# Kernel optimization log

Hardware: AMD Instinct MI355X
Metric: run time of the kernel (lower is better)

The kernel has to match this reference:

```python
import jax, jax.numpy as jnp
import numpy as np

EPS = 1e-5

def _conv(x, w, pad):
    # NCHW conv, stride 1, no bias
    return jax.lax.conv_general_dilated(x, w, (1, 1), [(pad, pad), (pad, pad)],
                                        dimension_numbers=('NCHW', 'OIHW', 'NCHW'))

def _bn(x, g, b, m, v):
    # inference-mode BatchNorm2d folded to scale/shift
    s = g * jax.lax.rsqrt(v + EPS)
    return x * s[None, :, None, None] + (b - m * s)[None, :, None, None]

def _cbr(x, w, g, b, m, v):
    # convolution helper module: 3x3 conv (pad 1, no bias) + BN + ReLU
    return jax.nn.relu(_bn(_conv(x, w, 1), g, b, m, v))


def setup_inputs() -> dict:
    key = jax.random.key(0)
    ks = iter(jax.random.split(key, 40))
    dim, mid, B, H, W = 256, 128, 4, 128, 128
    def conv_w(shape):
        fan = shape[1] * shape[2] * shape[3]
        return jax.random.normal(next(ks), shape, jnp.float32) / np.float32(np.sqrt(fan))
    def bn_p(c):
        return (jax.random.normal(next(ks), (c,), jnp.float32) * 0.1 + 1.0,
                jax.random.normal(next(ks), (c,), jnp.float32) * 0.1,
                jax.random.normal(next(ks), (c,), jnp.float32) * 0.1,
                jax.random.uniform(next(ks), (c,), jnp.float32, 0.5, 1.5))
    x = jax.random.normal(next(ks), (B, dim, H, W), jnp.float32)
    w_p1 = conv_w((mid, dim, 3, 3)); g_p1, b_p1, m_p1, v_p1 = bn_p(mid)
    w_p2 = conv_w((mid, dim, 3, 3)); g_p2, b_p2, m_p2, v_p2 = bn_p(mid)
    w_pc = conv_w((dim, mid, 3, 3)); g_pb, b_pb, m_pb, v_pb = bn_p(dim)
    w_c1 = conv_w((dim, dim, 1, 1)); g_b1, b_b1, m_b1, v_b1 = bn_p(dim)
    w_c2 = conv_w((dim, dim, 3, 3)); g_c2, b_c2, m_c2, v_c2 = bn_p(dim)
    return dict(x=x,
                w_p1=w_p1, g_p1=g_p1, b_p1=b_p1, m_p1=m_p1, v_p1=v_p1,
                w_p2=w_p2, g_p2=g_p2, b_p2=b_p2, m_p2=m_p2, v_p2=v_p2,
                w_pc=w_pc, g_pb=g_pb, b_pb=b_pb, m_pb=m_pb, v_pb=v_pb,
                w_c1=w_c1, g_b1=g_b1, b_b1=b_b1, m_b1=m_b1, v_b1=v_b1,
                w_c2=w_c2, g_c2=g_c2, b_c2=b_c2, m_c2=m_c2, v_c2=v_c2)


def reference(x, w_p1, g_p1, b_p1, m_p1, v_p1,
              w_p2, g_p2, b_p2, m_p2, v_p2,
              w_pc, g_pb, b_pb, m_pb, v_pb,
              w_c1, g_b1, b_b1, m_b1, v_b1,
              w_c2, g_c2, b_c2, m_c2, v_c2):
    p1 = _cbr(x, w_p1, g_p1, b_p1, m_p1, v_p1)          # [B,128,H,W]
    top = jax.lax.cummax(p1, axis=2, reverse=True)       # TopPool: max over rows below
    p2 = _cbr(x, w_p2, g_p2, b_p2, m_p2, v_p2)          # [B,128,H,W]
    left = jax.lax.cummax(p2, axis=3, reverse=True)      # LeftPool: max over cols to the right
    p_bn1 = _bn(_conv(top + left, w_pc, 1), g_pb, b_pb, m_pb, v_pb)  # [B,dim,H,W]
    bn1 = _bn(_conv(x, w_c1, 0), g_b1, b_b1, m_b1, v_b1)             # 1x1 skip branch
    relu1 = jax.nn.relu(p_bn1 + bn1)
    return _cbr(relu1, w_c2, g_c2, b_c2, m_c2, v_c2)
```

## Files before the change

### kernel.cpp

```cpp
#include <hip/hip_runtime.h>
#include <hip/hip_bf16.h>

#define HH 128
#define WW 128
#define BB 4
#define NPIX 16384
#define EPSV 1e-5f

using bfrag = __attribute__((ext_vector_type(8))) short;
using f32x4 = __attribute__((ext_vector_type(4))) float;
using us8   = __attribute__((ext_vector_type(8))) unsigned short;

__device__ __forceinline__ float bf2f(ushort u) {
  union { unsigned int i; float f; } x; x.i = ((unsigned int)u) << 16; return x.f;
}
__device__ __forceinline__ ushort f2bf(float f) {
  union { float f; unsigned int i; } x; x.f = f;
  unsigned int r = x.i + 0x7fffu + ((x.i >> 16) & 1u);
  return (ushort)(r >> 16);
}

#define GLOAD16(gsrc, ldst) \
  __builtin_amdgcn_global_load_lds( \
      (const __attribute__((address_space(1))) unsigned int*)(gsrc), \
      (__attribute__((address_space(3))) unsigned int*)(ldst), 16, 0, 0)

template<int CIN1, int TAPS1, int CIN2, int TAPS2, int COUT, int EPI>
__global__ __launch_bounds__(256, 2)
void convgemm(const ushort* __restrict__ B1,
              const ushort* __restrict__ B2,
              const ushort* __restrict__ wR,
              const float*  __restrict__ tb,
              const float*  __restrict__ tb2,
              void*          __restrict__ outp,
              const ushort* __restrict__ zerop)
{
  __shared__ ushort lds[2][16384];
  const int h      = blockIdx.x;
  const int o_base = blockIdx.y * 128;
  const int b      = blockIdx.z;
  const int tid  = threadIdx.x;
  const int lane = tid & 63;
  const int wid  = tid >> 6;
  const int m0 = (wid >> 1) * 64;
  const int n0 = (wid & 1) * 64;
  constexpr int nch1 = CIN1 / 64;
  constexpr int nch2 = (CIN2 > 0) ? CIN2 / 64 : 0;
  constexpr int NCH  = TAPS1 * nch1 + TAPS2 * nch2;

  f32x4 acc[4][4];
  #pragma unroll
  for (int i = 0; i < 4; ++i)
    #pragma unroll
    for (int j = 0; j < 4; ++j) acc[i][j] = (f32x4){0.f, 0.f, 0.f, 0.f};

  int rowB[4], ro1[4], ro2[4];
  #pragma unroll
  for (int s = 0; s < 4; ++s) {
    const int boff = (wid * 4 + s) * 1024 + lane * 16;
    rowB[s] = boff >> 7;
    const int sl8 = ((((boff >> 4) & 7) ^ (rowB[s] & 7)) << 3);
    ro1[s] = rowB[s] * CIN1 + sl8;
    ro2[s] = (CIN2 > 0) ? rowB[s] * CIN2 + sl8 : 0;
  }
  const size_t B1base = (size_t)b * NPIX * CIN1;
  const size_t B2base = (CIN2 > 0) ? (size_t)b * NPIX * CIN2 : 0;

  auto stage = [&](int t, int buf) {
    char* base = (char*)&lds[buf][0];
    const ushort* wsrc = wR + ((size_t)t * COUT + o_base) * 64;
    const ushort* bch;
    int zr; bool oob, ph2;
    if (CIN2 == 0 || t < TAPS1 * nch1) {
      const int tap = t / nch1, ch = t - tap * nch1;
      const int dy = (TAPS1 == 9) ? tap / 3 - 1 : 0;
      const int dx = (TAPS1 == 9) ? tap - (tap / 3) * 3 - 1 : 0;
      const int hy = h + dy;
      oob = (hy < 0) | (hy >= HH);
      zr  = (dx < 0) ? 0 : ((dx > 0) ? 127 : -1);
      bch = B1 + B1base + (size_t)(hy * WW + dx) * CIN1 + ch * 64;
      ph2 = false;
    } else {
      const int ch = t - TAPS1 * nch1;
      oob = false; zr = -1;
      bch = B2 + B2base + (size_t)(h * WW) * CIN2 + ch * 64;
      ph2 = true;
    }
    #pragma unroll
    for (int s = 0; s < 4; ++s) {
      const int off = (wid * 4 + s) * 1024;
      GLOAD16((const char*)wsrc + off + lane * 16, base + off);
      const int roff = ph2 ? ro2[s] : ro1[s];
      const ushort* bs = (oob || rowB[s] == zr) ? zerop : (bch + roff);
      GLOAD16(bs, base + 16384 + off);
    }
  };

  stage(0, 0);
  int cur = 0;
  for (int t = 0; t < NCH; ++t) {
    if (t + 1 < NCH) {
      stage(t + 1, cur ^ 1);
      asm volatile("s_waitcnt vmcnt(8)" ::: "memory");
    } else {
      asm volatile("s_waitcnt vmcnt(0)" ::: "memory");
    }
    __builtin_amdgcn_s_barrier();
    __builtin_amdgcn_sched_barrier(0);
    const char* base = (const char*)&lds[cur][0];
    __builtin_amdgcn_s_setprio(1);
    #pragma unroll
    for (int kc = 0; kc < 2; ++kc) {
      const int sw = ((((kc << 2) | (lane >> 4)) ^ (lane & 7)) << 4);
      bfrag af[4], bfv[4];
      #pragma unroll
      for (int mf = 0; mf < 4; ++mf)
        af[mf] = *(const bfrag*)(base + (m0 + mf * 16 + (lane & 15)) * 128 + sw);
      #pragma unroll
      for (int nf = 0; nf < 4; ++nf)
        bfv[nf] = *(const bfrag*)(base + 16384 + (n0 + nf * 16 + (lane & 15)) * 128 + sw);
      #pragma unroll
      for (int mf = 0; mf < 4; ++mf)
        #pragma unroll
        for (int nf = 0; nf < 4; ++nf)
          acc[mf][nf] = __builtin_amdgcn_mfma_f32_16x16x32_bf16(
              af[mf], bfv[nf], acc[mf][nf], 0, 0, 0);
    }
    __builtin_amdgcn_s_setprio(0);
    __builtin_amdgcn_sched_barrier(0);
    __builtin_amdgcn_s_barrier();
    cur ^= 1;
  }

  if (EPI == 4) {
    ushort* ct = (ushort*)&lds[0][0];
    const int pl0 = n0 + (lane & 15);
    #pragma unroll
    for (int mf = 0; mf < 4; ++mf) {
      #pragma unroll
      for (int r = 0; r < 4; ++r) {
        const int ol = m0 + mf * 16 + (lane >> 4) * 4 + r;
        const int o  = o_base + ol;
        const float bias = tb[o] + tb2[o];
        #pragma unroll
        for (int nf = 0; nf < 4; ++nf)
          ct[(pl0 + nf * 16) * 136 + ol] =
              f2bf(fmaxf(acc[mf][nf][r] + bias, 0.f));
      }
    }
    __syncthreads();
    const int p  = tid >> 1;
    const int hf = tid & 1;
    ushort* dst = (ushort*)outp +
                  ((size_t)b * NPIX + h * WW + p) * 256 + o_base + hf * 64;
    const ushort* src = ct + p * 136 + hf * 64;
    #pragma unroll
    for (int j = 0; j < 8; ++j)
      *(us8*)(dst + j * 8) = *(const us8*)(src + j * 8);
    return;
  }

  const int pc0 = h * WW + n0 + (lane & 15);
  #pragma unroll
  for (int mf = 0; mf < 4; ++mf) {
    #pragma unroll
    for (int r = 0; r < 4; ++r) {
      const int o = o_base + m0 + mf * 16 + (lane >> 4) * 4 + r;
      const float bias = tb[o];
      #pragma unroll
      for (int nf = 0; nf < 4; ++nf) {
        const int p = pc0 + nf * 16;
        float v = fmaxf(acc[mf][nf][r] + bias, 0.f);
        const size_t oi = ((size_t)(b * COUT + o)) * NPIX + p;
        if (EPI == 0) ((ushort*)outp)[oi] = f2bf(v);
        else          ((float*)outp)[oi] = v;
      }
    }
  }
}

struct WSeg {
  const float *W, *g, *bb, *mm, *vv;
  ushort* dst; float* tb;
  int CIN, COUT, TAPS, o_off, cb, start, end;
};

__device__ __forceinline__ void wrepack_one(const WSeg& s, int e) {
  const int tap = e % s.TAPS;
  const int ci  = (e / s.TAPS) % s.CIN;
  const int o   = e / (s.TAPS * s.CIN);
  const int oi  = o + s.o_off;
  const float sc = s.g[o] * rsqrtf(s.vv[o] + EPSV);
  const int nch = s.CIN / 64;
  const int ch = ci >> 6, kl = ci & 63;
  const int slot = (kl >> 3) ^ (oi & 7);
  s.dst[(((size_t)((s.cb + tap * nch + ch) * s.COUT) + oi) << 6) +
        (slot << 3) + (kl & 7)] = f2bf(s.W[e] * sc);
  if (ci == 0 && tap == 0) s.tb[oi] = s.bb[o] - s.mm[o] * sc;
}

__global__ __launch_bounds__(256)
void wrepack_all(WSeg s0, WSeg s1, WSeg s2, WSeg s3, WSeg s4) {
  const int id = blockIdx.x * 256 + threadIdx.x;
  if (id < s0.end)      wrepack_one(s0, id - s0.start);
  else if (id < s1.end) wrepack_one(s1, id - s1.start);
  else if (id < s2.end) wrepack_one(s2, id - s2.start);
  else if (id < s3.end) wrepack_one(s3, id - s3.start);
  else if (id < s4.end) wrepack_one(s4, id - s4.start);
}

__global__ __launch_bounds__(256)
void repack_x(const float* __restrict__ x, ushort* __restrict__ xT)
{
  const int b  = blockIdx.z;
  const int cq = threadIdx.x >> 6;
  const int pg = threadIdx.x & 63;
  const int p0 = blockIdx.x * 256 + pg * 4;
  const size_t xb = (size_t)b * 256 * NPIX;
  ushort* ob = xT + ((size_t)b * NPIX + p0) * 256 + cq * 64;
  for (int cc = 0; cc < 64; cc += 8) {
    us8 v[4];
    #pragma unroll
    for (int j = 0; j < 8; ++j) {
      const float4 q = *(const float4*)&x[xb + (size_t)(cq * 64 + cc + j) * NPIX + p0];
      v[0][j] = f2bf(q.x); v[1][j] = f2bf(q.y);
      v[2][j] = f2bf(q.z); v[3][j] = f2bf(q.w);
    }
    #pragma unroll
    for (int k = 0; k < 4; ++k)
      *(us8*)(ob + (size_t)k * 256 + cc) = v[k];
  }
}

__global__ __launch_bounds__(256)
void sum_repack(const ushort* __restrict__ p12, ushort* __restrict__ sT)
{
  const int b  = blockIdx.z;
  const int cq = threadIdx.x >> 6;
  const int pg = threadIdx.x & 63;
  const int p0 = blockIdx.x * 256 + pg * 4;
  const size_t base = (size_t)b * 256 * NPIX;
  const ushort* P1 = p12 + base;
  const ushort* P2 = p12 + base + (size_t)128 * NPIX;
  ushort* ob = sT + ((size_t)b * NPIX + p0) * 128 + cq * 32;
  for (int cc = 0; cc < 32; cc += 8) {
    us8 v[4];
    #pragma unroll
    for (int j = 0; j < 8; ++j) {
      const size_t ci = (size_t)(cq * 32 + cc + j) * NPIX + p0;
      const ushort4 a = *(const ushort4*)&P1[ci];
      const ushort4 d = *(const ushort4*)&P2[ci];
      v[0][j] = f2bf(bf2f(a.x) + bf2f(d.x));
      v[1][j] = f2bf(bf2f(a.y) + bf2f(d.y));
      v[2][j] = f2bf(bf2f(a.z) + bf2f(d.z));
      v[3][j] = f2bf(bf2f(a.w) + bf2f(d.w));
    }
    #pragma unroll
    for (int k = 0; k < 4; ++k)
      *(us8*)(ob + (size_t)k * 128 + cc) = v[k];
  }
}

__global__ __launch_bounds__(128)
void scan_h_rev(ushort* __restrict__ p, int co)
{
  const int bid = blockIdx.x;
  const int b = bid >> 7, c = bid & 127;
  ushort* base = p + ((size_t)(b * 256 + co + c)) * NPIX + threadIdx.x;
  float cur = bf2f(base[(HH - 1) * WW]);
  for (int hr = HH - 2; hr >= 0; --hr) {
    cur = fmaxf(cur, bf2f(base[hr * WW]));
    base[hr * WW] = f2bf(cur);
  }
}

__global__ __launch_bounds__(256)
void scan_w_rev(ushort* __restrict__ p, int co)
{
  const int lane = threadIdx.x & 63;
  const int rid  = blockIdx.x * 4 + (threadIdx.x >> 6);
  const int b = rid >> 14;
  const int rem = rid & 16383;
  const int c = rem >> 7, h = rem & 127;
  ushort* r = p + ((size_t)(b * 256 + co + c)) * NPIX + h * WW;
  const ushort2 u = ((const ushort2*)r)[lane];
  const float e0 = bf2f(u.x), e1 = bf2f(u.y);
  float m = fmaxf(e0, e1);
  #pragma unroll
  for (int off = 1; off < 64; off <<= 1) {
    const float o = __shfl_down(m, off, 64);
    if (lane + off < 64) m = fmaxf(m, o);
  }
  float s = __shfl_down(m, 1, 64);
  if (lane == 63) s = -3.4e38f;
  const float o1 = fmaxf(e1, s);
  const float o0 = fmaxf(e0, o1);
  ushort2 w; w.x = f2bf(o0); w.y = f2bf(o1);
  ((ushort2*)r)[lane] = w;
}

extern "C" void kernel_launch(void* const* d_in, const int* in_sizes, int n_in,
                              void* d_out, int out_size, void* d_ws, size_t ws_size,
                              hipStream_t stream) {
  const float* x    = (const float*)d_in[0];
  const float* w_p1 = (const float*)d_in[1];
  const float* g_p1 = (const float*)d_in[2];
  const float* b_p1 = (const float*)d_in[3];
  const float* m_p1 = (const float*)d_in[4];
  const float* v_p1 = (const float*)d_in[5];
  const float* w_p2 = (const float*)d_in[6];
  const float* g_p2 = (const float*)d_in[7];
  const float* b_p2 = (const float*)d_in[8];
  const float* m_p2 = (const float*)d_in[9];
  const float* v_p2 = (const float*)d_in[10];
  const float* w_pc = (const float*)d_in[11];
  const float* g_pb = (const float*)d_in[12];
  const float* b_pb = (const float*)d_in[13];
  const float* m_pb = (const float*)d_in[14];
  const float* v_pb = (const float*)d_in[15];
  const float* w_c1 = (const float*)d_in[16];
  const float* g_b1 = (const float*)d_in[17];
  const float* b_b1 = (const float*)d_in[18];
  const float* m_b1 = (const float*)d_in[19];
  const float* v_b1 = (const float*)d_in[20];
  const float* w_c2 = (const float*)d_in[21];
  const float* g_c2 = (const float*)d_in[22];
  const float* b_c2 = (const float*)d_in[23];
  const float* m_c2 = (const float*)d_in[24];
  const float* v_c2 = (const float*)d_in[25];

  char* ws = (char*)d_ws;
  ushort* xT      = (ushort*)(ws + 0);
  ushort* p12     = (ushort*)(ws + 33554432);
  ushort* relu1T  = (ushort*)(ws + 33554432);
  ushort* sumT    = (ushort*)(ws + 67108864);
  ushort* wR_p12  = (ushort*)(ws + 100663296);
  ushort* wR_pcc1 = (ushort*)(ws + 101842944);
  ushort* wR_c2   = (ushort*)(ws + 102563840);
  float*  tb_p12  = (float*)(ws + 103743488);
  float*  tb_pc   = (float*)(ws + 103744512);
  float*  tb_c1   = (float*)(ws + 103745536);
  float*  tb_c2   = (float*)(ws + 103746560);
  ushort* zerop   = (ushort*)(ws + 103747584);

  hipMemsetAsync(zerop, 0, 256, stream);

  const int n_p  = 128 * 256 * 9;
  const int n_pc = 256 * 128 * 9;
  const int n_c1 = 256 * 256 * 1;
  const int n_c2 = 256 * 256 * 9;
  WSeg s0 = {w_p1, g_p1, b_p1, m_p1, v_p1, wR_p12, tb_p12, 256, 256, 9, 0, 0,
             0, n_p};
  WSeg s1 = {w_p2, g_p2, b_p2, m_p2, v_p2, wR_p12, tb_p12, 256, 256, 9, 128, 0,
             n_p, 2 * n_p};
  WSeg s2 = {w_pc, g_pb, b_pb, m_pb, v_pb, wR_pcc1, tb_pc, 128, 256, 9, 0, 0,
             2 * n_p, 2 * n_p + n_pc};
  WSeg s3 = {w_c1, g_b1, b_b1, m_b1, v_b1, wR_pcc1, tb_c1, 256, 256, 1, 0, 18,
             2 * n_p + n_pc, 2 * n_p + n_pc + n_c1};
  WSeg s4 = {w_c2, g_c2, b_c2, m_c2, v_c2, wR_c2, tb_c2, 256, 256, 9, 0, 0,
             2 * n_p + n_pc + n_c1, 2 * n_p + n_pc + n_c1 + n_c2};
  const int n_all = 2 * n_p + n_pc + n_c1 + n_c2;
  wrepack_all<<<dim3((n_all + 255) / 256), 256, 0, stream>>>(s0, s1, s2, s3, s4);

  repack_x<<<dim3(NPIX / 256, 1, BB), 256, 0, stream>>>(x, xT);

  convgemm<256, 9, 0, 0, 256, 0><<<dim3(HH, 2, BB), 256, 0, stream>>>(
      xT, nullptr, wR_p12, tb_p12, nullptr, p12, zerop);

  scan_h_rev<<<dim3(BB * 128), 128, 0, stream>>>(p12, 0);
  scan_w_rev<<<dim3(BB * 128 * HH / 4), 256, 0, stream>>>(p12, 128);

  sum_repack<<<dim3(NPIX / 256, 1, BB), 256, 0, stream>>>(p12, sumT);

  convgemm<128, 9, 256, 1, 256, 4><<<dim3(HH, 2, BB), 256, 0, stream>>>(
      sumT, xT, wR_pcc1, tb_pc, tb_c1, relu1T, zerop);

  convgemm<256, 9, 0, 0, 256, 3><<<dim3(HH, 2, BB), 256, 0, stream>>>(
      relu1T, nullptr, wR_c2, tb_c2, nullptr, (void*)d_out, zerop);
}
```

Measured before the change: 316.5 us.

## Widen conv GEMM tile to all 256 outputs with 512 threads and triple buffering

Each block now computes all 256 output channels for one image row using 8 waves (512 threads), so the activation tile is loaded once rather than once per output-channel half. The LDS pipeline moves from double to triple buffering with a two-stage prefetch and a single barrier per step, and block indices are remapped so neighbouring blocks spread across XCDs. The cost is fewer, larger blocks (512 total) at one block per CU, 144KB of LDS per block, and a wider epilogue staging tile.

```diff
diff --git a/kernel.cpp b/kernel.cpp
--- a/kernel.cpp
+++ b/kernel.cpp
@@ -25,8 +25,8 @@
       (const __attribute__((address_space(1))) unsigned int*)(gsrc), \
       (__attribute__((address_space(3))) unsigned int*)(ldst), 16, 0, 0)
 
-template<int CIN1, int TAPS1, int CIN2, int TAPS2, int COUT, int EPI>
-__global__ __launch_bounds__(256, 2)
+template<int CIN1, int TAPS1, int CIN2, int TAPS2, int EPI>
+__global__ __launch_bounds__(512, 1)
 void convgemm(const ushort* __restrict__ B1,
               const ushort* __restrict__ B2,
               const ushort* __restrict__ wR,
@@ -35,18 +35,20 @@
               void*          __restrict__ outp,
               const ushort* __restrict__ zerop)
 {
-  __shared__ ushort lds[2][16384];
-  const int h      = blockIdx.x;
-  const int o_base = blockIdx.y * 128;
-  const int b      = blockIdx.z;
+  __shared__ char ldsb[3 * 49152];
+  constexpr int COUT = 256;
+  constexpr int nch1 = CIN1 / 64;
+  constexpr int nch2 = (CIN2 > 0) ? CIN2 / 64 : 0;
+  constexpr int NCH  = TAPS1 * nch1 + TAPS2 * nch2;
+
+  const int nid = (blockIdx.x & 7) * 64 + (blockIdx.x >> 3);
+  const int h = nid & 127;
+  const int b = nid >> 7;
   const int tid  = threadIdx.x;
   const int lane = tid & 63;
   const int wid  = tid >> 6;
   const int m0 = (wid >> 1) * 64;
   const int n0 = (wid & 1) * 64;
-  constexpr int nch1 = CIN1 / 64;
-  constexpr int nch2 = (CIN2 > 0) ? CIN2 / 64 : 0;
-  constexpr int NCH  = TAPS1 * nch1 + TAPS2 * nch2;
 
   f32x4 acc[4][4];
   #pragma unroll
@@ -54,10 +56,10 @@
     #pragma unroll
     for (int j = 0; j < 4; ++j) acc[i][j] = (f32x4){0.f, 0.f, 0.f, 0.f};
 
-  int rowB[4], ro1[4], ro2[4];
+  int rowB[2], ro1[2], ro2[2];
   #pragma unroll
-  for (int s = 0; s < 4; ++s) {
-    const int boff = (wid * 4 + s) * 1024 + lane * 16;
+  for (int s = 0; s < 2; ++s) {
+    const int boff = s * 8192 + tid * 16;
     rowB[s] = boff >> 7;
     const int sl8 = ((((boff >> 4) & 7) ^ (rowB[s] & 7)) << 3);
     ro1[s] = rowB[s] * CIN1 + sl8;
@@ -67,10 +69,13 @@
   const size_t B2base = (CIN2 > 0) ? (size_t)b * NPIX * CIN2 : 0;
 
   auto stage = [&](int t, int buf) {
-    char* base = (char*)&lds[buf][0];
-    const ushort* wsrc = wR + ((size_t)t * COUT + o_base) * 64;
-    const ushort* bch;
-    int zr; bool oob, ph2;
+    char* base = ldsb + buf * 49152;
+    const ushort* wsrc = wR + (size_t)t * (COUT * 64);
+    #pragma unroll
+    for (int s = 0; s < 4; ++s)
+      GLOAD16((const char*)wsrc + s * 8192 + tid * 16,
+              base + s * 8192 + tid * 16);
+    const ushort* bch; int zr; bool oob, ph2;
     if (CIN2 == 0 || t < TAPS1 * nch1) {
       const int tap = t / nch1, ch = t - tap * nch1;
       const int dy = (TAPS1 == 9) ? tap / 3 - 1 : 0;
@@ -87,27 +92,15 @@
       ph2 = true;
     }
     #pragma unroll
-    for (int s = 0; s < 4; ++s) {
-      const int off = (wid * 4 + s) * 1024;
-      GLOAD16((const char*)wsrc + off + lane * 16, base + off);
+    for (int s = 0; s < 2; ++s) {
       const int roff = ph2 ? ro2[s] : ro1[s];
       const ushort* bs = (oob || rowB[s] == zr) ? zerop : (bch + roff);
-      GLOAD16(bs, base + 16384 + off);
+      GLOAD16(bs, base + 32768 + s * 8192 + tid * 16);
     }
   };
 
-  stage(0, 0);
-  int cur = 0;
-  for (int t = 0; t < NCH; ++t) {
-    if (t + 1 < NCH) {
-      stage(t + 1, cur ^ 1);
-      asm volatile("s_waitcnt vmcnt(8)" ::: "memory");
-    } else {
-      asm volatile("s_waitcnt vmcnt(0)" ::: "memory");
-    }
-    __builtin_amdgcn_s_barrier();
-    __builtin_amdgcn_sched_barrier(0);
-    const char* base = (const char*)&lds[cur][0];
+  auto compute = [&](int buf) {
+    const char* base = ldsb + buf * 49152;
     __builtin_amdgcn_s_setprio(1);
     #pragma unroll
     for (int kc = 0; kc < 2; ++kc) {
@@ -118,7 +111,7 @@
         af[mf] = *(const bfrag*)(base + (m0 + mf * 16 + (lane & 15)) * 128 + sw);
       #pragma unroll
       for (int nf = 0; nf < 4; ++nf)
-        bfv[nf] = *(const bfrag*)(base + 16384 + (n0 + nf * 16 + (lane & 15)) * 128 + sw);
+        bfv[nf] = *(const bfrag*)(base + 32768 + (n0 + nf * 16 + (lane & 15)) * 128 + sw);
       #pragma unroll
       for (int mf = 0; mf < 4; ++mf)
         #pragma unroll
@@ -127,33 +120,47 @@
               af[mf], bfv[nf], acc[mf][nf], 0, 0, 0);
     }
     __builtin_amdgcn_s_setprio(0);
+  };
+
+  stage(0, 0);
+  stage(1, 1);
+  int cur = 0, nxt = 2;
+  for (int t = 0; t < NCH - 1; ++t) {
+    asm volatile("s_waitcnt vmcnt(6)" ::: "memory");
+    __builtin_amdgcn_s_barrier();
     __builtin_amdgcn_sched_barrier(0);
-    __builtin_amdgcn_s_barrier();
-    cur ^= 1;
-  }
+    if (t + 2 < NCH) stage(t + 2, nxt);
+    compute(cur);
+    cur = (cur == 2) ? 0 : cur + 1;
+    nxt = (nxt == 2) ? 0 : nxt + 1;
+  }
+  asm volatile("s_waitcnt vmcnt(0)" ::: "memory");
+  __builtin_amdgcn_s_barrier();
+  __builtin_amdgcn_sched_barrier(0);
+  compute(cur);
 
   if (EPI == 4) {
-    ushort* ct = (ushort*)&lds[0][0];
+    __syncthreads();
+    ushort* ct = (ushort*)ldsb;
     const int pl0 = n0 + (lane & 15);
     #pragma unroll
     for (int mf = 0; mf < 4; ++mf) {
       #pragma unroll
       for (int r = 0; r < 4; ++r) {
-        const int ol = m0 + mf * 16 + (lane >> 4) * 4 + r;
-        const int o  = o_base + ol;
+        const int o = m0 + mf * 16 + (lane >> 4) * 4 + r;
         const float bias = tb[o] + tb2[o];
         #pragma unroll
         for (int nf = 0; nf < 4; ++nf)
-          ct[(pl0 + nf * 16) * 136 + ol] =
+          ct[(pl0 + nf * 16) * 264 + o] =
               f2bf(fmaxf(acc[mf][nf][r] + bias, 0.f));
       }
     }
     __syncthreads();
-    const int p  = tid >> 1;
-    const int hf = tid & 1;
+    const int p = tid >> 2;
+    const int q = tid & 3;
     ushort* dst = (ushort*)outp +
-                  ((size_t)b * NPIX + h * WW + p) * 256 + o_base + hf * 64;
-    const ushort* src = ct + p * 136 + hf * 64;
+                  ((size_t)b * NPIX + h * WW + p) * 256 + q * 64;
+    const ushort* src = ct + p * 264 + q * 64;
     #pragma unroll
     for (int j = 0; j < 8; ++j)
       *(us8*)(dst + j * 8) = *(const us8*)(src + j * 8);
@@ -165,13 +172,13 @@
   for (int mf = 0; mf < 4; ++mf) {
     #pragma unroll
     for (int r = 0; r < 4; ++r) {
-      const int o = o_base + m0 + mf * 16 + (lane >> 4) * 4 + r;
+      const int o = m0 + mf * 16 + (lane >> 4) * 4 + r;
       const float bias = tb[o];
       #pragma unroll
       for (int nf = 0; nf < 4; ++nf) {
         const int p = pc0 + nf * 16;
         float v = fmaxf(acc[mf][nf][r] + bias, 0.f);
-        const size_t oi = ((size_t)(b * COUT + o)) * NPIX + p;
+        const size_t oi = ((size_t)(b * 256 + o)) * NPIX + p;
         if (EPI == 0) ((ushort*)outp)[oi] = f2bf(v);
         else          ((float*)outp)[oi] = v;
       }
@@ -364,7 +371,7 @@
 
   repack_x<<<dim3(NPIX / 256, 1, BB), 256, 0, stream>>>(x, xT);
 
-  convgemm<256, 9, 0, 0, 256, 0><<<dim3(HH, 2, BB), 256, 0, stream>>>(
+  convgemm<256, 9, 0, 0, 0><<<dim3(HH * BB), 512, 0, stream>>>(
       xT, nullptr, wR_p12, tb_p12, nullptr, p12, zerop);
 
   scan_h_rev<<<dim3(BB * 128), 128, 0, stream>>>(p12, 0);
@@ -372,9 +379,9 @@
 
   sum_repack<<<dim3(NPIX / 256, 1, BB), 256, 0, stream>>>(p12, sumT);
 
-  convgemm<128, 9, 256, 1, 256, 4><<<dim3(HH, 2, BB), 256, 0, stream>>>(
+  convgemm<128, 9, 256, 1, 4><<<dim3(HH * BB), 512, 0, stream>>>(
       sumT, xT, wR_pcc1, tb_pc, tb_c1, relu1T, zerop);
 
-  convgemm<256, 9, 0, 0, 256, 3><<<dim3(HH, 2, BB), 256, 0, stream>>>(
+  convgemm<256, 9, 0, 0, 3><<<dim3(HH * BB), 512, 0, stream>>>(
       relu1T, nullptr, wR_c2, tb_c2, nullptr, (void*)d_out, zerop);
 }
```

Measured after the change: 323.4 us. 2.2% more time.

## Remap conv grid for XCD locality, restructure K-loop pipeline, merge scan kernels

Applied to the files above, without the earlier changes.

Block indices in the conv GEMMs are remapped from a 3D grid to a 1D grid, so that consecutive blocks landing on the same XCD (blockIdx & 7) work on contiguous row groups. This aims to improve L2 reuse of the overlapping 3x3 input rows and of the weights. The main loop now waits for all loads with vmcnt(0) and a single barrier, then issues the next stage's prefetch before computing, and LDS fragment loads for both k-chunks are hoisted ahead of the MFMAs. The two pooling scan kernels are merged into one launch to save a launch. The new loop drops the trailing barrier and waits on all outstanding loads, which may reduce load/compute overlap.

```diff
diff --git a/kernel.cpp b/kernel.cpp
--- a/kernel.cpp
+++ b/kernel.cpp
@@ -25,7 +25,7 @@
       (const __attribute__((address_space(1))) unsigned int*)(gsrc), \
       (__attribute__((address_space(3))) unsigned int*)(ldst), 16, 0, 0)
 
-template<int CIN1, int TAPS1, int CIN2, int TAPS2, int COUT, int EPI>
+template<int CIN1, int TAPS1, int CIN2, int TAPS2, int EPI>
 __global__ __launch_bounds__(256, 2)
 void convgemm(const ushort* __restrict__ B1,
               const ushort* __restrict__ B2,
@@ -36,17 +36,22 @@
               const ushort* __restrict__ zerop)
 {
   __shared__ ushort lds[2][16384];
-  const int h      = blockIdx.x;
-  const int o_base = blockIdx.y * 128;
-  const int b      = blockIdx.z;
+  constexpr int nch1 = CIN1 / 64;
+  constexpr int nch2 = (CIN2 > 0) ? CIN2 / 64 : 0;
+  constexpr int NCH  = TAPS1 * nch1 + TAPS2 * nch2;
+
+  const int g  = blockIdx.x & 7;
+  const int r  = blockIdx.x >> 3;
+  const int bo = r >> 4;
+  const int h  = g * 16 + (r & 15);
+  const int o_base = (bo & 1) * 128;
+  const int b  = bo >> 1;
+
   const int tid  = threadIdx.x;
   const int lane = tid & 63;
   const int wid  = tid >> 6;
   const int m0 = (wid >> 1) * 64;
   const int n0 = (wid & 1) * 64;
-  constexpr int nch1 = CIN1 / 64;
-  constexpr int nch2 = (CIN2 > 0) ? CIN2 / 64 : 0;
-  constexpr int NCH  = TAPS1 * nch1 + TAPS2 * nch2;
 
   f32x4 acc[4][4];
   #pragma unroll
@@ -68,7 +73,7 @@
 
   auto stage = [&](int t, int buf) {
     char* base = (char*)&lds[buf][0];
-    const ushort* wsrc = wR + ((size_t)t * COUT + o_base) * 64;
+    const ushort* wsrc = wR + ((size_t)t * 256 + o_base) * 64;
     const ushort* bch;
     int zr; bool oob, ph2;
     if (CIN2 == 0 || t < TAPS1 * nch1) {
@@ -96,56 +101,57 @@
     }
   };
 
-  stage(0, 0);
-  int cur = 0;
-  for (int t = 0; t < NCH; ++t) {
-    if (t + 1 < NCH) {
-      stage(t + 1, cur ^ 1);
-      asm volatile("s_waitcnt vmcnt(8)" ::: "memory");
-    } else {
-      asm volatile("s_waitcnt vmcnt(0)" ::: "memory");
-    }
-    __builtin_amdgcn_s_barrier();
-    __builtin_amdgcn_sched_barrier(0);
-    const char* base = (const char*)&lds[cur][0];
-    __builtin_amdgcn_s_setprio(1);
+  auto compute = [&](int buf) {
+    const char* base = (const char*)&lds[buf][0];
+    bfrag af[2][4], bfv[2][4];
     #pragma unroll
     for (int kc = 0; kc < 2; ++kc) {
       const int sw = ((((kc << 2) | (lane >> 4)) ^ (lane & 7)) << 4);
-      bfrag af[4], bfv[4];
       #pragma unroll
       for (int mf = 0; mf < 4; ++mf)
-        af[mf] = *(const bfrag*)(base + (m0 + mf * 16 + (lane & 15)) * 128 + sw);
+        af[kc][mf] = *(const bfrag*)(base + (m0 + mf * 16 + (lane & 15)) * 128 + sw);
       #pragma unroll
       for (int nf = 0; nf < 4; ++nf)
-        bfv[nf] = *(const bfrag*)(base + 16384 + (n0 + nf * 16 + (lane & 15)) * 128 + sw);
+        bfv[kc][nf] = *(const bfrag*)(base + 16384 + (n0 + nf * 16 + (lane & 15)) * 128 + sw);
+    }
+    __builtin_amdgcn_s_setprio(1);
+    #pragma unroll
+    for (int kc = 0; kc < 2; ++kc)
       #pragma unroll
       for (int mf = 0; mf < 4; ++mf)
         #pragma unroll
         for (int nf = 0; nf < 4; ++nf)
           acc[mf][nf] = __builtin_amdgcn_mfma_f32_16x16x32_bf16(
-              af[mf], bfv[nf], acc[mf][nf], 0, 0, 0);
-    }
+              af[kc][mf], bfv[kc][nf], acc[mf][nf], 0, 0, 0);
     __builtin_amdgcn_s_setprio(0);
+  };
+
+  stage(0, 0);
+  int cur = 0;
+  for (int t = 0; t < NCH; ++t) {
+    asm volatile("s_waitcnt vmcnt(0)" ::: "memory");
+    __builtin_amdgcn_s_barrier();
     __builtin_amdgcn_sched_barrier(0);
-    __builtin_amdgcn_s_barrier();
+    if (t + 1 < NCH) stage(t + 1, cur ^ 1);
+    compute(cur);
     cur ^= 1;
   }
 
   if (EPI == 4) {
+    __syncthreads();
     ushort* ct = (ushort*)&lds[0][0];
     const int pl0 = n0 + (lane & 15);
     #pragma unroll
     for (int mf = 0; mf < 4; ++mf) {
       #pragma unroll
-      for (int r = 0; r < 4; ++r) {
-        const int ol = m0 + mf * 16 + (lane >> 4) * 4 + r;
+      for (int r2 = 0; r2 < 4; ++r2) {
+        const int ol = m0 + mf * 16 + (lane >> 4) * 4 + r2;
         const int o  = o_base + ol;
         const float bias = tb[o] + tb2[o];
         #pragma unroll
         for (int nf = 0; nf < 4; ++nf)
           ct[(pl0 + nf * 16) * 136 + ol] =
-              f2bf(fmaxf(acc[mf][nf][r] + bias, 0.f));
+              f2bf(fmaxf(acc[mf][nf][r2] + bias, 0.f));
       }
     }
     __syncthreads();
@@ -164,14 +170,14 @@
   #pragma unroll
   for (int mf = 0; mf < 4; ++mf) {
     #pragma unroll
-    for (int r = 0; r < 4; ++r) {
-      const int o = o_base + m0 + mf * 16 + (lane >> 4) * 4 + r;
+    for (int r2 = 0; r2 < 4; ++r2) {
+      const int o = o_base + m0 + mf * 16 + (lane >> 4) * 4 + r2;
       const float bias = tb[o];
       #pragma unroll
       for (int nf = 0; nf < 4; ++nf) {
         const int p = pc0 + nf * 16;
-        float v = fmaxf(acc[mf][nf][r] + bias, 0.f);
-        const size_t oi = ((size_t)(b * COUT + o)) * NPIX + p;
+        float v = fmaxf(acc[mf][nf][r2] + bias, 0.f);
+        const size_t oi = ((size_t)(b * 256 + o)) * NPIX + p;
         if (EPI == 0) ((ushort*)outp)[oi] = f2bf(v);
         else          ((float*)outp)[oi] = v;
       }
@@ -261,42 +267,42 @@
   }
 }
 
-__global__ __launch_bounds__(128)
-void scan_h_rev(ushort* __restrict__ p, int co)
+__global__ __launch_bounds__(256)
+void scans(ushort* __restrict__ p)
 {
   const int bid = blockIdx.x;
-  const int b = bid >> 7, c = bid & 127;
-  ushort* base = p + ((size_t)(b * 256 + co + c)) * NPIX + threadIdx.x;
-  float cur = bf2f(base[(HH - 1) * WW]);
-  for (int hr = HH - 2; hr >= 0; --hr) {
-    cur = fmaxf(cur, bf2f(base[hr * WW]));
-    base[hr * WW] = f2bf(cur);
-  }
-}
-
-__global__ __launch_bounds__(256)
-void scan_w_rev(ushort* __restrict__ p, int co)
-{
-  const int lane = threadIdx.x & 63;
-  const int rid  = blockIdx.x * 4 + (threadIdx.x >> 6);
-  const int b = rid >> 14;
-  const int rem = rid & 16383;
-  const int c = rem >> 7, h = rem & 127;
-  ushort* r = p + ((size_t)(b * 256 + co + c)) * NPIX + h * WW;
-  const ushort2 u = ((const ushort2*)r)[lane];
-  const float e0 = bf2f(u.x), e1 = bf2f(u.y);
-  float m = fmaxf(e0, e1);
-  #pragma unroll
-  for (int off = 1; off < 64; off <<= 1) {
-    const float o = __shfl_down(m, off, 64);
-    if (lane + off < 64) m = fmaxf(m, o);
-  }
-  float s = __shfl_down(m, 1, 64);
-  if (lane == 63) s = -3.4e38f;
-  const float o1 = fmaxf(e1, s);
-  const float o0 = fmaxf(e0, o1);
-  ushort2 w; w.x = f2bf(o0); w.y = f2bf(o1);
-  ((ushort2*)r)[lane] = w;
+  if (bid < 256) {
+    const int b = bid >> 6;
+    const int c = (bid & 63) * 2 + (threadIdx.x >> 7);
+    const int w = threadIdx.x & 127;
+    ushort* base = p + ((size_t)(b * 256 + c)) * NPIX + w;
+    float cur = bf2f(base[(HH - 1) * WW]);
+    for (int hr = HH - 2; hr >= 0; --hr) {
+      cur = fmaxf(cur, bf2f(base[hr * WW]));
+      base[hr * WW] = f2bf(cur);
+    }
+  } else {
+    const int lane = threadIdx.x & 63;
+    const int rid  = (bid - 256) * 4 + (threadIdx.x >> 6);
+    const int b = rid >> 14;
+    const int rem = rid & 16383;
+    const int c = rem >> 7, h = rem & 127;
+    ushort* r = p + ((size_t)(b * 256 + 128 + c)) * NPIX + h * WW;
+    const ushort2 u = ((const ushort2*)r)[lane];
+    const float e0 = bf2f(u.x), e1 = bf2f(u.y);
+    float m = fmaxf(e0, e1);
+    #pragma unroll
+    for (int off = 1; off < 64; off <<= 1) {
+      const float o = __shfl_down(m, off, 64);
+      if (lane + off < 64) m = fmaxf(m, o);
+    }
+    float s = __shfl_down(m, 1, 64);
+    if (lane == 63) s = -3.4e38f;
+    const float o1 = fmaxf(e1, s);
+    const float o0 = fmaxf(e0, o1);
+    ushort2 w2; w2.x = f2bf(o0); w2.y = f2bf(o1);
+    ((ushort2*)r)[lane] = w2;
+  }
 }
 
 extern "C" void kernel_launch(void* const* d_in, const int* in_sizes, int n_in,
@@ -364,17 +370,16 @@
 
   repack_x<<<dim3(NPIX / 256, 1, BB), 256, 0, stream>>>(x, xT);
 
-  convgemm<256, 9, 0, 0, 256, 0><<<dim3(HH, 2, BB), 256, 0, stream>>>(
+  convgemm<256, 9, 0, 0, 0><<<dim3(1024), 256, 0, stream>>>(
       xT, nullptr, wR_p12, tb_p12, nullptr, p12, zerop);
 
-  scan_h_rev<<<dim3(BB * 128), 128, 0, stream>>>(p12, 0);
-  scan_w_rev<<<dim3(BB * 128 * HH / 4), 256, 0, stream>>>(p12, 128);
+  scans<<<dim3(256 + 16384), 256, 0, stream>>>(p12);
 
   sum_repack<<<dim3(NPIX / 256, 1, BB), 256, 0, stream>>>(p12, sumT);
 
-  convgemm<128, 9, 256, 1, 256, 4><<<dim3(HH, 2, BB), 256, 0, stream>>>(
+  convgemm<128, 9, 256, 1, 4><<<dim3(1024), 256, 0, stream>>>(
       sumT, xT, wR_pcc1, tb_pc, tb_c1, relu1T, zerop);
 
-  convgemm<256, 9, 0, 0, 256, 3><<<dim3(HH, 2, BB), 256, 0, stream>>>(
+  convgemm<256, 9, 0, 0, 3><<<dim3(1024), 256, 0, stream>>>(
       relu1T, nullptr, wR_c2, tb_c2, nullptr, (void*)d_out, zerop);
 }
```

After: 300.2 us. -5.2%, faster.
